# Performance work log

Measured on AMD Instinct MI355X. Metric: run time of the kernel, lower is better.

## Reference

```python
import jax, jax.numpy as jnp
import numpy as np

BINS = 100
ALPHA = 0.1

def entropy_batch(h):
    # Faithful to torch: histogram path is detached (done in numpy in original).
    h = jax.lax.stop_gradient(h)
    B, D = h.shape
    hp = h - jnp.min(h, axis=1, keepdims=True)
    hn = hp / jnp.max(hp, axis=1, keepdims=True)  # normalized to [0, 1]
    # np.histogram with `bins` uniform bins over [0,1]; rightmost edge inclusive -> clip
    idx = jnp.clip(jnp.floor(hn * BINS).astype(jnp.int32), 0, BINS - 1)
    rows = jnp.arange(B)[:, None]
    counts = jnp.zeros((B, BINS), jnp.float32).at[rows, idx].add(1.0)
    px = counts / jnp.float32(D)
    safe = jnp.where(px > 0, px, 1.0)
    ent = -jnp.sum(px * jnp.log(safe), axis=1) + jnp.log(jnp.float32(BINS))
    return jnp.mean(ent)

def setup_inputs() -> dict:
    key = jax.random.key(0)
    ks = jax.random.split(key, 8)
    B = 65536
    archi = [246, 246, 246, 246, 246, 246]
    dims = [784] + archi
    inp = {"x": jax.random.normal(ks[0], (B, 1, 28, 28), jnp.float32)}
    for i in range(6):
        inp[f"W{i+1}"] = 0.01 * jax.random.normal(ks[i + 1], (dims[i + 1], dims[i]), jnp.float32)
        inp[f"b{i+1}"] = jnp.zeros((dims[i + 1],), jnp.float32)
    inp["W7"] = 0.01 * jax.random.normal(ks[7], (10, archi[-1]), jnp.float32)
    inp["b7"] = jnp.zeros((10,), jnp.float32)
    return inp

def reference(x, W1, b1, W2, b2, W3, b3, W4, b4, W5, b5, W6, b6, W7, b7):
    h = x.reshape(-1, 784)
    Hs = []
    for W, b in ((W1, b1), (W2, b2), (W3, b3), (W4, b4), (W5, b5), (W6, b6)):
        h = jax.nn.leaky_relu(h @ W.T + b, negative_slope=ALPHA)
        Hs.append(entropy_batch(h))
    logits = jax.nn.relu(h @ W7.T + b7)
    out = jax.nn.log_softmax(logits, axis=1)
    return (out, Hs[0], Hs[1], Hs[2], Hs[3], Hs[4], Hs[5])
```

## Files before the change

### kernel.cpp

```cpp
#include <hip/hip_runtime.h>
#include <cstdint>
#include <cmath>

#define BATCH 65536
#define NREAL 246
#define NPAD  256
#define K1    784
#define K1PAD 832
#define BINS  100
#define ALPHA 0.1f
#define RB    32
#define NBLK  (BATCH/RB)

typedef __bf16 bf16x8 __attribute__((ext_vector_type(8)));
typedef __bf16 bf16x4 __attribute__((ext_vector_type(4)));
typedef __bf16 bf16x2 __attribute__((ext_vector_type(2)));
typedef float  f32x4  __attribute__((ext_vector_type(4)));

#define OFF_HS     0
#define OFF_STAGE  16384
#define OFF_HIST   16384
#define OFF_MN     29184
#define OFF_MX     30208
#define OFF_WENT   31232
#define LDS_TOTAL  31424

__global__ __launch_bounds__(256)
void pad_weights(const float* __restrict__ W1, const float* __restrict__ W2,
                 const float* __restrict__ W3, const float* __restrict__ W4,
                 const float* __restrict__ W5, const float* __restrict__ W6,
                 const float* __restrict__ W7,
                 const float* __restrict__ b1, const float* __restrict__ b2,
                 const float* __restrict__ b3, const float* __restrict__ b4,
                 const float* __restrict__ b5, const float* __restrict__ b6,
                 __bf16* __restrict__ W1p, __bf16* __restrict__ Wp,
                 __bf16* __restrict__ W7p, float* __restrict__ bpad)
{
    int tid = blockIdx.x * 256 + threadIdx.x;
    const int n1 = NPAD * K1PAD;
    const int n2 = 5 * NPAD * NPAD;
    const int n3 = 16 * NPAD;
    if (tid < n1) {
        int row = tid / K1PAD;
        int k   = tid - row * K1PAD;
        W1p[tid] = (__bf16)((row < NREAL && k < K1) ? W1[row * K1 + k] : 0.0f);
    } else if (tid < n1 + n2) {
        int t = tid - n1;
        int wsel = t >> 16;
        int idx  = t & 65535;
        int row  = idx >> 8, k = idx & 255;
        const float* W = (wsel == 0) ? W2 : (wsel == 1) ? W3 : (wsel == 2) ? W4
                        : (wsel == 3) ? W5 : W6;
        Wp[t] = (__bf16)((row < NREAL && k < NREAL) ? W[row * NREAL + k] : 0.0f);
    } else if (tid < n1 + n2 + n3) {
        int t = tid - n1 - n2;
        int row = t >> 8, k = t & 255;
        W7p[t] = (__bf16)((row < 10 && k < NREAL) ? W7[row * NREAL + k] : 0.0f);
    } else if (tid < n1 + n2 + n3 + 6 * NPAD) {
        int t = tid - n1 - n2 - n3;
        int li = t >> 8, k = t & 255;
        const float* b = (li == 0) ? b1 : (li == 1) ? b2 : (li == 2) ? b3
                        : (li == 3) ? b4 : (li == 4) ? b5 : b6;
        bpad[t] = (k < NREAL) ? b[k] : 0.0f;
    }
}

__global__ __launch_bounds__(512)
void mega(const float* __restrict__ x,
          const __bf16* __restrict__ W1p,
          const __bf16* __restrict__ Wp,
          const __bf16* __restrict__ W7p,
          const float* __restrict__ bpad,
          const float* __restrict__ b7,
          float* __restrict__ out, float* __restrict__ partial)
{
    __shared__ char smem[LDS_TOTAL];
    char*  Hb    = smem + OFF_HS;
    float* rowmn = (float*)(smem + OFF_MN);
    float* rowmx = (float*)(smem + OFF_MX);
    float* went  = (float*)(smem + OFF_WENT);
    int*   hist  = (int*)(smem + OFF_HIST);

    const int tid = threadIdx.x;
    const int w = tid >> 6, l = tid & 63;
    const int lane16 = l & 15, lane4 = l >> 4;
    const int wc = w * 32;
    const int m0 = blockIdx.x * RB;

    const int rg = l >> 4, q = l & 15;
    const int erow = w * 4 + rg;
    const int eswz = (erow & 7) << 4;
    int* histW = hist + w * 400;

    f32x4 acc[2][2];
#pragma unroll
    for (int i = 0; i < 2; ++i)
#pragma unroll
        for (int j = 0; j < 2; ++j) acc[i][j] = f32x4{0.f, 0.f, 0.f, 0.f};

    bf16x8 Bq[2][2];

    auto loadBq = [&](int s, const __bf16* Bbase, int hh) {
        const __bf16* pp = Bbase + (size_t)(wc + lane16) * NPAD + hh * 32 + lane4 * 8;
#pragma unroll
        for (int j = 0; j < 2; ++j)
            Bq[s][j] = *(const bf16x8*)(pp + (size_t)j * 16 * NPAD);
    };

    auto epilogue = [&](const float* bp) {
        f32x4 bq[2];
#pragma unroll
        for (int j = 0; j < 2; ++j)
            bq[j] = *(const f32x4*)(bp + wc + j * 16 + lane4 * 4);
#pragma unroll
        for (int i = 0; i < 2; ++i) {
            const int m = i * 16 + lane16;
            const int swz = (m & 7) << 4;
            float mn = 1e30f, mx = -1e30f;
#pragma unroll
            for (int j = 0; j < 2; ++j) {
                const int nbase = wc + j * 16 + lane4 * 4;
                bf16x4 hv;
#pragma unroll
                for (int r = 0; r < 4; ++r) {
                    float v = acc[i][j][r] + bq[j][r];
                    v = v > 0.0f ? v : ALPHA * v;
                    bool valid = (nbase + r) < NREAL;
                    hv[r] = valid ? (__bf16)v : (__bf16)0.0f;
                    float vb = (float)hv[r];
                    mn = fminf(mn, valid ? vb : 1e30f);
                    mx = fmaxf(mx, valid ? vb : -1e30f);
                }
                *(bf16x4*)(Hb + m * 512 + ((nbase * 2) ^ swz)) = hv;
            }
            mn = fminf(mn, __shfl_xor(mn, 16, 64));
            mx = fmaxf(mx, __shfl_xor(mx, 16, 64));
            mn = fminf(mn, __shfl_xor(mn, 32, 64));
            mx = fmaxf(mx, __shfl_xor(mx, 32, 64));
            if (lane4 == 0) { rowmn[m * 8 + w] = mn; rowmx[m * 8 + w] = mx; }
        }
    };

    auto esum = [&](int li) {
        const int* hrow = histW + rg * 100;
        float S = 0.0f;
#pragma unroll
        for (int t = 0; t < 7; ++t) {
            int b = q * 7 + t;
            if (b < 100) {
                float f = (float)hrow[b];
                float g = fmaxf(f, 1.0f);
                S = fmaf(f, __logf(g), S);
            }
        }
#pragma unroll
        for (int off = 1; off < 64; off <<= 1) S += __shfl_xor(S, off, 64);
        if (l == 0) went[w * 6 + li] = 4.0f * logf(246.0f) - S * (1.0f / 246.0f);
    };

    {
        const int srow = tid >> 4;
        const int skc  = (tid & 15) * 4;
        float4 xr;
        auto issueX = [&](int kt) {
            int k0 = kt * 64 + skc;
            if (k0 < K1) {
                xr = *(const float4*)(x + (size_t)(m0 + srow) * K1 + k0);
            } else {
                xr = float4{0.f, 0.f, 0.f, 0.f};
            }
        };
        auto writeX = [&](int buf) {
            bf16x4 h;
            h[0]=(__bf16)xr.x; h[1]=(__bf16)xr.y; h[2]=(__bf16)xr.z; h[3]=(__bf16)xr.w;
            char* st = smem + OFF_STAGE + buf * 4096;
            *(bf16x4*)(st + srow * 128 + ((skc * 2) ^ ((srow & 7) << 4))) = h;
        };
        auto lB = [&](int s, int kt, int kk) {
            const __bf16* p = W1p + (size_t)(wc + lane16) * K1PAD + kt * 64 + kk * 32 + lane4 * 8;
#pragma unroll
            for (int j = 0; j < 2; ++j)
                Bq[s][j] = *(const bf16x8*)(p + (size_t)j * 16 * K1PAD);
        };
        auto cH = [&](const char* st, int kbyte, int s) {
#pragma unroll
            for (int i = 0; i < 2; ++i) {
                int m = i * 16 + lane16;
                bf16x8 af = *(const bf16x8*)(st + m * 128 + ((kbyte + lane4 * 16) ^ ((m & 7) << 4)));
                __builtin_amdgcn_s_setprio(1);
#pragma unroll
                for (int j = 0; j < 2; ++j)
                    acc[i][j] = __builtin_amdgcn_mfma_f32_16x16x32_bf16(s ? Bq[1][j] : Bq[0][j], af, acc[i][j], 0, 0, 0);
                __builtin_amdgcn_s_setprio(0);
            }
        };

        issueX(0); writeX(0); issueX(1);
        lB(0, 0, 0);
        for (int kt = 0; kt < 13; ++kt) {
            __syncthreads();
            if (kt < 12) { writeX((kt + 1) & 1); if (kt < 11) issueX(kt + 2); }
            const char* st = smem + OFF_STAGE + (kt & 1) * 4096;
            lB(1, kt, 1);
            cH(st, 0, 0);
            if (kt < 12) lB(0, kt + 1, 0);
            cH(st, 64, 1);
        }
    }

    loadBq(0, Wp, 0);
    loadBq(1, Wp, 1);
    epilogue(bpad);
    __syncthreads();

    for (int p = 0; p < 5; ++p) {
        const __bf16* WpP = Wp + (size_t)p * (NPAD * NPAD);
        const __bf16* WpN = WpP + NPAD * NPAD;

#pragma unroll
        for (int i = 0; i < 2; ++i)
#pragma unroll
            for (int j = 0; j < 2; ++j) acc[i][j] = f32x4{0.f, 0.f, 0.f, 0.f};

#pragma unroll
        for (int t = 0; t < 7; ++t) { int b = t * 64 + l; if (b < 400) histW[b] = 0; }
        f32x4 m4 = *(const f32x4*)(rowmn + erow * 8);
        f32x4 m5 = *(const f32x4*)(rowmn + erow * 8 + 4);
        f32x4 x4 = *(const f32x4*)(rowmx + erow * 8);
        f32x4 x5 = *(const f32x4*)(rowmx + erow * 8 + 4);
        float emn = fminf(fminf(fminf(m4[0], m4[1]), fminf(m4[2], m4[3])),
                          fminf(fminf(m5[0], m5[1]), fminf(m5[2], m5[3])));
        float emx = fmaxf(fmaxf(fmaxf(x4[0], x4[1]), fmaxf(x4[2], x4[3])),
                          fmaxf(fmaxf(x5[0], x5[1]), fmaxf(x5[2], x5[3])));
        float ers = (emx > emn) ? 100.0f / (emx - emn) : 0.0f;
        float eb  = -emn * ers;
        asm volatile("s_waitcnt lgkmcnt(0)" ::: "memory");

#pragma unroll
        for (int h = 0; h < 8; ++h) {
#pragma unroll
            for (int i = 0; i < 2; ++i) {
                int m = i * 16 + lane16;
                bf16x8 af = *(const bf16x8*)(Hb + m * 512 + ((h * 64 + lane4 * 16) ^ ((m & 7) << 4)));
                __builtin_amdgcn_s_setprio(1);
#pragma unroll
                for (int j = 0; j < 2; ++j)
                    acc[i][j] = __builtin_amdgcn_mfma_f32_16x16x32_bf16((h & 1) ? Bq[1][j] : Bq[0][j],
                                                                        af, acc[i][j], 0, 0, 0);
                __builtin_amdgcn_s_setprio(0);
            }
            if (h < 6)      loadBq(h & 1, WpP, h + 2);
            else if (p < 4) loadBq(h & 1, WpN, h - 6);
            {
                int c0 = q * 16 + h * 2;
                bf16x2 hv = *(const bf16x2*)(Hb + erow * 512 + ((c0 * 2) ^ eswz));
#pragma unroll
                for (int e = 0; e < 2; ++e) {
                    if (c0 + e < NREAL) {
                        int idx = (int)fmaf((float)hv[e], ers, eb);
                        idx = idx > BINS - 1 ? BINS - 1 : (idx < 0 ? 0 : idx);
                        atomicAdd(&histW[rg * 100 + idx], 1);
                    }
                }
            }
        }
        asm volatile("s_waitcnt lgkmcnt(0)" ::: "memory");
        esum(p);

        __syncthreads();
        epilogue(bpad + (size_t)(p + 1) * NPAD);
        __syncthreads();
    }

    {
#pragma unroll
        for (int t = 0; t < 7; ++t) { int b = t * 64 + l; if (b < 400) histW[b] = 0; }
        f32x4 m4 = *(const f32x4*)(rowmn + erow * 8);
        f32x4 m5 = *(const f32x4*)(rowmn + erow * 8 + 4);
        f32x4 x4 = *(const f32x4*)(rowmx + erow * 8);
        f32x4 x5 = *(const f32x4*)(rowmx + erow * 8 + 4);
        float emn = fminf(fminf(fminf(m4[0], m4[1]), fminf(m4[2], m4[3])),
                          fminf(fminf(m5[0], m5[1]), fminf(m5[2], m5[3])));
        float emx = fmaxf(fmaxf(fmaxf(x4[0], x4[1]), fmaxf(x4[2], x4[3])),
                          fmaxf(fmaxf(x5[0], x5[1]), fmaxf(x5[2], x5[3])));
        float ers = (emx > emn) ? 100.0f / (emx - emn) : 0.0f;
        float eb  = -emn * ers;
        asm volatile("s_waitcnt lgkmcnt(0)" ::: "memory");
#pragma unroll
        for (int h = 0; h < 8; ++h) {
            int c0 = q * 16 + h * 2;
            bf16x2 hv = *(const bf16x2*)(Hb + erow * 512 + ((c0 * 2) ^ eswz));
#pragma unroll
            for (int e = 0; e < 2; ++e) {
                if (c0 + e < NREAL) {
                    int idx = (int)fmaf((float)hv[e], ers, eb);
                    idx = idx > BINS - 1 ? BINS - 1 : (idx < 0 ? 0 : idx);
                    atomicAdd(&histW[rg * 100 + idx], 1);
                }
            }
        }
        asm volatile("s_waitcnt lgkmcnt(0)" ::: "memory");
        esum(5);
    }

    if (w < 2) {
        f32x4 hacc = f32x4{0.f, 0.f, 0.f, 0.f};
        int row = w * 16 + lane16;
#pragma unroll
        for (int kt = 0; kt < 8; ++kt) {
            bf16x8 af = *(const bf16x8*)(Hb + row * 512 + ((kt * 64 + lane4 * 16) ^ ((row & 7) << 4)));
            bf16x8 bf = *(const bf16x8*)(W7p + (size_t)lane16 * NPAD + kt * 32 + lane4 * 8);
            hacc = __builtin_amdgcn_mfma_f32_16x16x32_bf16(af, bf, hacc, 0, 0, 0);
        }
        float bv = (lane16 < 10) ? b7[lane16] : 0.0f;
#pragma unroll
        for (int r = 0; r < 4; ++r) {
            float lg = fmaxf(hacc[r] + bv, 0.0f);
            float vm = (lane16 < 10) ? lg : -1e30f;
#pragma unroll
            for (int off = 8; off; off >>= 1) vm = fmaxf(vm, __shfl_xor(vm, off, 64));
            float ex = (lane16 < 10) ? expf(lg - vm) : 0.0f;
#pragma unroll
            for (int off = 8; off; off >>= 1) ex += __shfl_xor(ex, off, 64);
            float ls = vm + logf(ex);
            if (lane16 < 10) {
                int grow = m0 + w * 16 + lane4 * 4 + r;
                out[(size_t)grow * 10 + lane16] = lg - ls;
            }
        }
    }

    __syncthreads();
    if (tid < 6) {
        float s = 0.0f;
#pragma unroll
        for (int qq = 0; qq < 8; ++qq) s += went[qq * 6 + tid];
        partial[tid * NBLK + blockIdx.x] = s;
    }
}

__global__ __launch_bounds__(256)
void reduce_kernel(const float* __restrict__ partial, float* __restrict__ out)
{
    __shared__ float s[256];
    const int li = blockIdx.x, tid = threadIdx.x;
    float a = 0.0f;
    for (int i = tid; i < NBLK; i += 256) a += partial[li * NBLK + i];
    s[tid] = a;
    __syncthreads();
    for (int st = 128; st; st >>= 1) {
        if (tid < st) s[tid] += s[tid + st];
        __syncthreads();
    }
    if (tid == 0)
        out[(size_t)BATCH * 10 + li] = s[0] / (float)BATCH + logf((float)BINS);
}

extern "C" void kernel_launch(void* const* d_in, const int* in_sizes, int n_in,
                              void* d_out, int out_size, void* d_ws, size_t ws_size,
                              hipStream_t stream)
{
    (void)in_sizes; (void)n_in; (void)out_size; (void)ws_size;

    const float* x  = (const float*)d_in[0];
    const float* W1 = (const float*)d_in[1];
    const float* b1 = (const float*)d_in[2];
    const float* W2 = (const float*)d_in[3];
    const float* b2 = (const float*)d_in[4];
    const float* W3 = (const float*)d_in[5];
    const float* b3 = (const float*)d_in[6];
    const float* W4 = (const float*)d_in[7];
    const float* b4 = (const float*)d_in[8];
    const float* W5 = (const float*)d_in[9];
    const float* b5 = (const float*)d_in[10];
    const float* W6 = (const float*)d_in[11];
    const float* b6 = (const float*)d_in[12];
    const float* W7 = (const float*)d_in[13];
    const float* b7 = (const float*)d_in[14];

    char* ws = (char*)d_ws;
    __bf16* W1p = (__bf16*)(ws);
    __bf16* Wp  = (__bf16*)(ws + 425984);
    __bf16* W7p = (__bf16*)(ws + 1081344);
    float*  bpad = (float*)(ws + 1089536);
    float*  partial = (float*)(ws + 1095680);
    float*  out = (float*)d_out;

    pad_weights<<<2134, 256, 0, stream>>>(W1, W2, W3, W4, W5, W6, W7,
                                          b1, b2, b3, b4, b5, b6,
                                          W1p, Wp, W7p, bpad);
    mega<<<NBLK, 512, 0, stream>>>(x, W1p, Wp, W7p, bpad, b7, out, partial);
    reduce_kernel<<<6, 256, 0, stream>>>(partial, out);
}
```

Baseline: 290.4 us.

## Double-buffer hidden activations to drop one barrier per layer and batch histogram work

```diff
diff --git a/kernel.cpp b/kernel.cpp
--- a/kernel.cpp
+++ b/kernel.cpp
@@ -14,16 +14,15 @@
 
 typedef __bf16 bf16x8 __attribute__((ext_vector_type(8)));
 typedef __bf16 bf16x4 __attribute__((ext_vector_type(4)));
-typedef __bf16 bf16x2 __attribute__((ext_vector_type(2)));
 typedef float  f32x4  __attribute__((ext_vector_type(4)));
 
 #define OFF_HS     0
-#define OFF_STAGE  16384
-#define OFF_HIST   16384
-#define OFF_MN     29184
-#define OFF_MX     30208
-#define OFF_WENT   31232
-#define LDS_TOTAL  31424
+#define OFF_STAGE  32768
+#define OFF_HIST   32768
+#define OFF_MN     45568
+#define OFF_MX     47616
+#define OFF_WENT   49664
+#define LDS_TOTAL  49856
 
 __global__ __launch_bounds__(256)
 void pad_weights(const float* __restrict__ W1, const float* __restrict__ W2,
@@ -75,11 +74,10 @@
           float* __restrict__ out, float* __restrict__ partial)
 {
     __shared__ char smem[LDS_TOTAL];
-    char*  Hb    = smem + OFF_HS;
+    char*  Hball = smem + OFF_HS;
     float* rowmn = (float*)(smem + OFF_MN);
     float* rowmx = (float*)(smem + OFF_MX);
     float* went  = (float*)(smem + OFF_WENT);
-    int*   hist  = (int*)(smem + OFF_HIST);
 
     const int tid = threadIdx.x;
     const int w = tid >> 6, l = tid & 63;
@@ -90,7 +88,7 @@
     const int rg = l >> 4, q = l & 15;
     const int erow = w * 4 + rg;
     const int eswz = (erow & 7) << 4;
-    int* histW = hist + w * 400;
+    int* histW = (int*)(smem + OFF_HIST) + w * 400;
 
     f32x4 acc[2][2];
 #pragma unroll
@@ -107,37 +105,109 @@
             Bq[s][j] = *(const bf16x8*)(pp + (size_t)j * 16 * NPAD);
     };
 
-    auto epilogue = [&](const float* bp) {
-        f32x4 bq[2];
-#pragma unroll
-        for (int j = 0; j < 2; ++j)
-            bq[j] = *(const f32x4*)(bp + wc + j * 16 + lane4 * 4);
+    auto zeroHist = [&]() {
+        int4* hz = (int4*)histW;
+        const int4 z = int4{0, 0, 0, 0};
+        hz[l] = z;
+        if (l < 36) hz[64 + l] = z;
+    };
+
+    auto gemmLayer = [&](const char* Hs_, const __bf16* WpP, const __bf16* WpN) {
+#pragma unroll
+        for (int i = 0; i < 2; ++i)
+#pragma unroll
+            for (int j = 0; j < 2; ++j) acc[i][j] = f32x4{0.f, 0.f, 0.f, 0.f};
+        const int sw0 = (lane16 & 7) << 4;
+#pragma unroll
+        for (int h = 0; h < 8; ++h) {
+            bf16x8 af0 = *(const bf16x8*)(Hs_ + (lane16) * 512      + ((h * 64 + lane4 * 16) ^ sw0));
+            bf16x8 af1 = *(const bf16x8*)(Hs_ + (16 + lane16) * 512 + ((h * 64 + lane4 * 16) ^ sw0));
+            __builtin_amdgcn_s_setprio(1);
+            acc[0][0] = __builtin_amdgcn_mfma_f32_16x16x32_bf16((h & 1) ? Bq[1][0] : Bq[0][0], af0, acc[0][0], 0, 0, 0);
+            acc[0][1] = __builtin_amdgcn_mfma_f32_16x16x32_bf16((h & 1) ? Bq[1][1] : Bq[0][1], af0, acc[0][1], 0, 0, 0);
+            acc[1][0] = __builtin_amdgcn_mfma_f32_16x16x32_bf16((h & 1) ? Bq[1][0] : Bq[0][0], af1, acc[1][0], 0, 0, 0);
+            acc[1][1] = __builtin_amdgcn_mfma_f32_16x16x32_bf16((h & 1) ? Bq[1][1] : Bq[0][1], af1, acc[1][1], 0, 0, 0);
+            __builtin_amdgcn_s_setprio(0);
+            if (h < 6)           loadBq(h & 1, WpP, h + 2);
+            else if (WpN != nullptr) loadBq(h & 1, WpN, h - 6);
+        }
+    };
+
+    auto entropyBurst = [&](const char* Hs_, int sbuf) {
+        f32x4 a0 = *(const f32x4*)(rowmn + sbuf * 256 + erow * 8);
+        f32x4 a1 = *(const f32x4*)(rowmn + sbuf * 256 + erow * 8 + 4);
+        f32x4 b0 = *(const f32x4*)(rowmx + sbuf * 256 + erow * 8);
+        f32x4 b1 = *(const f32x4*)(rowmx + sbuf * 256 + erow * 8 + 4);
+        f32x4 mnv = __builtin_elementwise_min(a0, a1);
+        f32x4 mxv = __builtin_elementwise_max(b0, b1);
+        float emn = fminf(fminf(mnv[0], mnv[1]), fminf(mnv[2], mnv[3]));
+        float emx = fmaxf(fmaxf(mxv[0], mxv[1]), fmaxf(mxv[2], mxv[3]));
+        float ers = (emx > emn) ? 100.0f / (emx - emn) : 0.0f;
+        float eb  = -emn * ers;
+        bf16x8 h0 = *(const bf16x8*)(Hs_ + erow * 512 + ((q * 32) ^ eswz));
+        bf16x8 h1 = *(const bf16x8*)(Hs_ + erow * 512 + ((q * 32 + 16) ^ eswz));
+        int* hrow = histW + rg * 100;
+#pragma unroll
+        for (int e = 0; e < 8; ++e) {
+            int c = q * 16 + e;
+            if (c < NREAL) {
+                int idx = (int)fmaf((float)h0[e], ers, eb);
+                idx = idx > BINS - 1 ? BINS - 1 : (idx < 0 ? 0 : idx);
+                atomicAdd(&hrow[idx], 1);
+            }
+        }
+#pragma unroll
+        for (int e = 0; e < 8; ++e) {
+            int c = q * 16 + 8 + e;
+            if (c < NREAL) {
+                int idx = (int)fmaf((float)h1[e], ers, eb);
+                idx = idx > BINS - 1 ? BINS - 1 : (idx < 0 ? 0 : idx);
+                atomicAdd(&hrow[idx], 1);
+            }
+        }
+    };
+
+    auto epilogue = [&](f32x4 bq0, f32x4 bq1, char* Hd, int dbuf) {
+        const f32x4 zero = f32x4{0.f, 0.f, 0.f, 0.f};
 #pragma unroll
         for (int i = 0; i < 2; ++i) {
             const int m = i * 16 + lane16;
             const int swz = (m & 7) << 4;
-            float mn = 1e30f, mx = -1e30f;
+            f32x4 mn4 = f32x4{1e30f, 1e30f, 1e30f, 1e30f};
+            f32x4 mx4 = f32x4{-1e30f, -1e30f, -1e30f, -1e30f};
 #pragma unroll
             for (int j = 0; j < 2; ++j) {
                 const int nbase = wc + j * 16 + lane4 * 4;
+                f32x4 v = acc[i][j] + (j ? bq1 : bq0);
+                f32x4 lk = __builtin_elementwise_max(v, zero)
+                         + ALPHA * __builtin_elementwise_min(v, zero);
                 bf16x4 hv;
-#pragma unroll
-                for (int r = 0; r < 4; ++r) {
-                    float v = acc[i][j][r] + bq[j][r];
-                    v = v > 0.0f ? v : ALPHA * v;
-                    bool valid = (nbase + r) < NREAL;
-                    hv[r] = valid ? (__bf16)v : (__bf16)0.0f;
-                    float vb = (float)hv[r];
-                    mn = fminf(mn, valid ? vb : 1e30f);
-                    mx = fmaxf(mx, valid ? vb : -1e30f);
+                if (nbase + 4 <= NREAL) {
+#pragma unroll
+                    for (int r = 0; r < 4; ++r) hv[r] = (__bf16)lk[r];
+                    mn4 = __builtin_elementwise_min(mn4, lk);
+                    mx4 = __builtin_elementwise_max(mx4, lk);
+                } else {
+#pragma unroll
+                    for (int r = 0; r < 4; ++r) {
+                        bool valid = (nbase + r) < NREAL;
+                        hv[r] = valid ? (__bf16)lk[r] : (__bf16)0.0f;
+                        mn4[r] = fminf(mn4[r], valid ? lk[r] : 1e30f);
+                        mx4[r] = fmaxf(mx4[r], valid ? lk[r] : -1e30f);
+                    }
                 }
-                *(bf16x4*)(Hb + m * 512 + ((nbase * 2) ^ swz)) = hv;
-            }
+                *(bf16x4*)(Hd + m * 512 + ((nbase * 2) ^ swz)) = hv;
+            }
+            float mn = fminf(fminf(mn4[0], mn4[1]), fminf(mn4[2], mn4[3]));
+            float mx = fmaxf(fmaxf(mx4[0], mx4[1]), fmaxf(mx4[2], mx4[3]));
             mn = fminf(mn, __shfl_xor(mn, 16, 64));
             mx = fmaxf(mx, __shfl_xor(mx, 16, 64));
             mn = fminf(mn, __shfl_xor(mn, 32, 64));
             mx = fmaxf(mx, __shfl_xor(mx, 32, 64));
-            if (lane4 == 0) { rowmn[m * 8 + w] = mn; rowmx[m * 8 + w] = mx; }
+            if (lane4 == 0) {
+                rowmn[dbuf * 256 + m * 8 + w] = mn;
+                rowmx[dbuf * 256 + m * 8 + w] = mx;
+            }
         }
     };
 
@@ -210,105 +280,41 @@
 
     loadBq(0, Wp, 0);
     loadBq(1, Wp, 1);
-    epilogue(bpad);
+    {
+        f32x4 bq0 = *(const f32x4*)(bpad + wc + lane4 * 4);
+        f32x4 bq1 = *(const f32x4*)(bpad + wc + 16 + lane4 * 4);
+        epilogue(bq0, bq1, Hball, 0);
+    }
     __syncthreads();
+    zeroHist();
 
     for (int p = 0; p < 5; ++p) {
+        const char* Hs_ = Hball + (p & 1) * 16384;
+        char*       Hd  = Hball + ((p & 1) ^ 1) * 16384;
         const __bf16* WpP = Wp + (size_t)p * (NPAD * NPAD);
-        const __bf16* WpN = WpP + NPAD * NPAD;
-
-#pragma unroll
-        for (int i = 0; i < 2; ++i)
-#pragma unroll
-            for (int j = 0; j < 2; ++j) acc[i][j] = f32x4{0.f, 0.f, 0.f, 0.f};
-
-#pragma unroll
-        for (int t = 0; t < 7; ++t) { int b = t * 64 + l; if (b < 400) histW[b] = 0; }
-        f32x4 m4 = *(const f32x4*)(rowmn + erow * 8);
-        f32x4 m5 = *(const f32x4*)(rowmn + erow * 8 + 4);
-        f32x4 x4 = *(const f32x4*)(rowmx + erow * 8);
-        f32x4 x5 = *(const f32x4*)(rowmx + erow * 8 + 4);
-        float emn = fminf(fminf(fminf(m4[0], m4[1]), fminf(m4[2], m4[3])),
-                          fminf(fminf(m5[0], m5[1]), fminf(m5[2], m5[3])));
-        float emx = fmaxf(fmaxf(fmaxf(x4[0], x4[1]), fmaxf(x4[2], x4[3])),
-                          fmaxf(fmaxf(x5[0], x5[1]), fmaxf(x5[2], x5[3])));
-        float ers = (emx > emn) ? 100.0f / (emx - emn) : 0.0f;
-        float eb  = -emn * ers;
-        asm volatile("s_waitcnt lgkmcnt(0)" ::: "memory");
-
-#pragma unroll
-        for (int h = 0; h < 8; ++h) {
-#pragma unroll
-            for (int i = 0; i < 2; ++i) {
-                int m = i * 16 + lane16;
-                bf16x8 af = *(const bf16x8*)(Hb + m * 512 + ((h * 64 + lane4 * 16) ^ ((m & 7) << 4)));
-                __builtin_amdgcn_s_setprio(1);
-#pragma unroll
-                for (int j = 0; j < 2; ++j)
-                    acc[i][j] = __builtin_amdgcn_mfma_f32_16x16x32_bf16((h & 1) ? Bq[1][j] : Bq[0][j],
-                                                                        af, acc[i][j], 0, 0, 0);
-                __builtin_amdgcn_s_setprio(0);
-            }
-            if (h < 6)      loadBq(h & 1, WpP, h + 2);
-            else if (p < 4) loadBq(h & 1, WpN, h - 6);
-            {
-                int c0 = q * 16 + h * 2;
-                bf16x2 hv = *(const bf16x2*)(Hb + erow * 512 + ((c0 * 2) ^ eswz));
-#pragma unroll
-                for (int e = 0; e < 2; ++e) {
-                    if (c0 + e < NREAL) {
-                        int idx = (int)fmaf((float)hv[e], ers, eb);
-                        idx = idx > BINS - 1 ? BINS - 1 : (idx < 0 ? 0 : idx);
-                        atomicAdd(&histW[rg * 100 + idx], 1);
-                    }
-                }
-            }
-        }
+
+        gemmLayer(Hs_, WpP, (p < 4) ? WpP + NPAD * NPAD : nullptr);
+        f32x4 bq0 = *(const f32x4*)(bpad + (size_t)(p + 1) * NPAD + wc + lane4 * 4);
+        f32x4 bq1 = *(const f32x4*)(bpad + (size_t)(p + 1) * NPAD + wc + 16 + lane4 * 4);
+        entropyBurst(Hs_, p & 1);
+        epilogue(bq0, bq1, Hd, (p & 1) ^ 1);
         asm volatile("s_waitcnt lgkmcnt(0)" ::: "memory");
         esum(p);
-
+        zeroHist();
         __syncthreads();
-        epilogue(bpad + (size_t)(p + 1) * NPAD);
-        __syncthreads();
-    }
-
-    {
-#pragma unroll
-        for (int t = 0; t < 7; ++t) { int b = t * 64 + l; if (b < 400) histW[b] = 0; }
-        f32x4 m4 = *(const f32x4*)(rowmn + erow * 8);
-        f32x4 m5 = *(const f32x4*)(rowmn + erow * 8 + 4);
-        f32x4 x4 = *(const f32x4*)(rowmx + erow * 8);
-        f32x4 x5 = *(const f32x4*)(rowmx + erow * 8 + 4);
-        float emn = fminf(fminf(fminf(m4[0], m4[1]), fminf(m4[2], m4[3])),
-                          fminf(fminf(m5[0], m5[1]), fminf(m5[2], m5[3])));
-        float emx = fmaxf(fmaxf(fmaxf(x4[0], x4[1]), fmaxf(x4[2], x4[3])),
-                          fmaxf(fmaxf(x5[0], x5[1]), fmaxf(x5[2], x5[3])));
-        float ers = (emx > emn) ? 100.0f / (emx - emn) : 0.0f;
-        float eb  = -emn * ers;
-        asm volatile("s_waitcnt lgkmcnt(0)" ::: "memory");
-#pragma unroll
-        for (int h = 0; h < 8; ++h) {
-            int c0 = q * 16 + h * 2;
-            bf16x2 hv = *(const bf16x2*)(Hb + erow * 512 + ((c0 * 2) ^ eswz));
-#pragma unroll
-            for (int e = 0; e < 2; ++e) {
-                if (c0 + e < NREAL) {
-                    int idx = (int)fmaf((float)hv[e], ers, eb);
-                    idx = idx > BINS - 1 ? BINS - 1 : (idx < 0 ? 0 : idx);
-                    atomicAdd(&histW[rg * 100 + idx], 1);
-                }
-            }
-        }
-        asm volatile("s_waitcnt lgkmcnt(0)" ::: "memory");
-        esum(5);
-    }
+    }
+
+    entropyBurst(Hball + 16384, 1);
+    asm volatile("s_waitcnt lgkmcnt(0)" ::: "memory");
+    esum(5);
 
     if (w < 2) {
+        const char* H6 = Hball + 16384;
         f32x4 hacc = f32x4{0.f, 0.f, 0.f, 0.f};
         int row = w * 16 + lane16;
 #pragma unroll
         for (int kt = 0; kt < 8; ++kt) {
-            bf16x8 af = *(const bf16x8*)(Hb + row * 512 + ((kt * 64 + lane4 * 16) ^ ((row & 7) << 4)));
+            bf16x8 af = *(const bf16x8*)(H6 + row * 512 + ((kt * 64 + lane4 * 16) ^ ((row & 7) << 4)));
             bf16x8 bf = *(const bf16x8*)(W7p + (size_t)lane16 * NPAD + kt * 32 + lane4 * 8);
             hacc = __builtin_amdgcn_mfma_f32_16x16x32_bf16(af, bf, hacc, 0, 0, 0);
         }
```

Result: no change. 291.0 us (+0.2%).
